# Kernel tuning notes

Measured on AMD Instinct MI355X. Metric: run time of the kernel, lower is better.

Reference implementation:

```python
import jax, jax.numpy as jnp
import numpy as np

B, S, D = 8, 1024, 1024
H = 16
HD = D // H  # 64
FF = 4 * D   # 4096
EPS = 1e-5


def layer_norm(x, g, b):
    mu = jnp.mean(x, axis=-1, keepdims=True)
    var = jnp.mean(jnp.square(x - mu), axis=-1, keepdims=True)
    return (x - mu) * jax.lax.rsqrt(var + EPS) * g + b


def setup_inputs() -> dict:
    key = jax.random.key(0)
    ks = jax.random.split(key, 16)
    s_in = 1.0 / np.sqrt(D)
    s_ff = 1.0 / np.sqrt(FF)
    return {
        "x": jax.random.normal(ks[0], (B, S, D), jnp.float32),
        "ln1_g": jnp.ones((D,), jnp.float32),
        "ln1_b": jnp.zeros((D,), jnp.float32),
        "ln2_g": jnp.ones((D,), jnp.float32),
        "ln2_b": jnp.zeros((D,), jnp.float32),
        # per-head projections stacked on a leading head axis: [H, D, HD]
        "Wq": jax.random.uniform(ks[1], (H, D, HD), jnp.float32, -s_in, s_in),
        "bq": jax.random.uniform(ks[2], (H, HD), jnp.float32, -s_in, s_in),
        "Wk": jax.random.uniform(ks[3], (H, D, HD), jnp.float32, -s_in, s_in),
        "bk": jax.random.uniform(ks[4], (H, HD), jnp.float32, -s_in, s_in),
        "Wv": jax.random.uniform(ks[5], (H, D, HD), jnp.float32, -s_in, s_in),
        "bv": jax.random.uniform(ks[6], (H, HD), jnp.float32, -s_in, s_in),
        "Wo": jax.random.uniform(ks[7], (D, D), jnp.float32, -s_in, s_in),
        "bo": jax.random.uniform(ks[8], (D,), jnp.float32, -s_in, s_in),
        "W1": jax.random.uniform(ks[9], (D, FF), jnp.float32, -s_in, s_in),
        "b1": jax.random.uniform(ks[10], (FF,), jnp.float32, -s_in, s_in),
        "W2": jax.random.uniform(ks[11], (FF, D), jnp.float32, -s_ff, s_ff),
        "b2": jax.random.uniform(ks[12], (D,), jnp.float32, -s_ff, s_ff),
    }


def attention(h, Wq, bq, Wk, bk, Wv, bv, Wo, bo):
    # h: [B,S,D] -> q/k/v: [B,H,S,HD]
    q = jnp.einsum("bsd,hdk->bhsk", h, Wq) + bq[None, :, None, :]
    k = jnp.einsum("bsd,hdk->bhsk", h, Wk) + bk[None, :, None, :]
    v = jnp.einsum("bsd,hdk->bhsk", h, Wv) + bv[None, :, None, :]
    scores = jnp.einsum("bhsk,bhtk->bhst", q, k) / jnp.sqrt(jnp.float32(HD))
    w = jax.nn.softmax(scores, axis=-1)  # [B,H,S,S]
    o = jnp.einsum("bhst,bhtk->bhsk", w, v)
    # concat heads (head order matches torch.cat over per-head outputs)
    o = o.transpose(0, 2, 1, 3).reshape(h.shape[0], h.shape[1], D)
    return o @ Wo + bo


def reference(x, ln1_g, ln1_b, ln2_g, ln2_b, Wq, bq, Wk, bk, Wv, bv, Wo, bo, W1, b1, W2, b2):
    h = layer_norm(x, ln1_g, ln1_b)
    x = x + attention(h, Wq, bq, Wk, bk, Wv, bv, Wo, bo)
    h2 = layer_norm(x, ln2_g, ln2_b)
    ff = jax.nn.gelu(h2 @ W1 + b1, approximate=False) @ W2 + b2  # dropout in eval = identity
    return x + ff
```

## Files before the change

### kernel.cpp

```cpp
#include <hip/hip_runtime.h>
#include <hip/hip_bf16.h>
#include <math.h>

#define DMODEL 1024
#define NH     16
#define HD     64
#define FFDIM  4096
#define SEQ    1024
#define BATCH  8
#define ROWS   (BATCH * SEQ)

typedef __bf16 bf16x8 __attribute__((ext_vector_type(8)));
typedef __bf16 bf16x4 __attribute__((ext_vector_type(4)));
typedef float  f32x4  __attribute__((ext_vector_type(4)));

__device__ __forceinline__ unsigned short f2bf(float f) {
  unsigned int u = __builtin_bit_cast(unsigned int, f);
  u += 0x7fff + ((u >> 16) & 1);
  return (unsigned short)(u >> 16);
}

__device__ __forceinline__ void gload_lds16(const void* g, void* l) {
  __builtin_amdgcn_global_load_lds(
      (const __attribute__((address_space(1))) unsigned int*)g,
      (__attribute__((address_space(3))) unsigned int*)l, 16, 0, 0);
}

__device__ __forceinline__ bf16x8 tr_read8(const unsigned short* p) {
  bf16x4 lo, hi;
  const __attribute__((address_space(3))) unsigned short* p3 =
      (const __attribute__((address_space(3))) unsigned short*)p;
  asm volatile("ds_read_b64_tr_b16 %0, %2\n\t"
               "ds_read_b64_tr_b16 %1, %2 offset:128"
               : "=v"(lo), "=v"(hi)
               : "v"(p3));
  return __builtin_shufflevector(lo, hi, 0, 1, 2, 3, 4, 5, 6, 7);
}

__global__ __launch_bounds__(256) void ln_bf16_kernel(
    const float* __restrict__ x, const float* __restrict__ g,
    const float* __restrict__ bta, unsigned short* __restrict__ out) {
  int row = blockIdx.x;
  int tid = threadIdx.x;
  int wid = tid >> 6, lane = tid & 63;
  const float4 v = ((const float4*)(x + (size_t)row * DMODEL))[tid];
  float s = v.x + v.y + v.z + v.w;
#pragma unroll
  for (int off = 32; off >= 1; off >>= 1) s += __shfl_xor(s, off, 64);
  __shared__ float red[8];
  if (lane == 0) red[wid] = s;
  __syncthreads();
  float mu = (red[0] + red[1] + red[2] + red[3]) * (1.0f / DMODEL);
  float4 d;
  d.x = v.x - mu; d.y = v.y - mu; d.z = v.z - mu; d.w = v.w - mu;
  float sq = d.x * d.x + d.y * d.y + d.z * d.z + d.w * d.w;
#pragma unroll
  for (int off = 32; off >= 1; off >>= 1) sq += __shfl_xor(sq, off, 64);
  if (lane == 0) red[4 + wid] = sq;
  __syncthreads();
  float var = (red[4] + red[5] + red[6] + red[7]) * (1.0f / DMODEL);
  float rs = rsqrtf(var + 1e-5f);
  const float4 gg = ((const float4*)g)[tid];
  const float4 bb = ((const float4*)bta)[tid];
  ushort4 o;
  o.x = f2bf(d.x * rs * gg.x + bb.x);
  o.y = f2bf(d.y * rs * gg.y + bb.y);
  o.z = f2bf(d.z * rs * gg.z + bb.z);
  o.w = f2bf(d.w * rs * gg.w + bb.w);
  ((ushort4*)(out + (size_t)row * DMODEL))[tid] = o;
}

__global__ __launch_bounds__(256) void transpose_f2b_kernel(
    const float* __restrict__ in, unsigned short* __restrict__ out,
    int R, int C, long long ibs, long long obs) {
  __shared__ float tile[64][65];
  int b = blockIdx.z;
  int r0 = blockIdx.y * 64, c0 = blockIdx.x * 64;
  const float* ip = in + (size_t)b * ibs;
  unsigned short* op = out + (size_t)b * obs;
  int tid = threadIdx.x;
  int rl = tid >> 4, cl = (tid & 15) * 4;
#pragma unroll
  for (int it = 0; it < 4; ++it) {
    int r = it * 16 + rl;
    float4 v = *(const float4*)(ip + (size_t)(r0 + r) * C + c0 + cl);
    tile[r][cl] = v.x; tile[r][cl + 1] = v.y;
    tile[r][cl + 2] = v.z; tile[r][cl + 3] = v.w;
  }
  __syncthreads();
#pragma unroll
  for (int it = 0; it < 4; ++it) {
    int c = it * 16 + rl;
    ushort4 o;
    o.x = f2bf(tile[cl + 0][c]); o.y = f2bf(tile[cl + 1][c]);
    o.z = f2bf(tile[cl + 2][c]); o.w = f2bf(tile[cl + 3][c]);
    *(ushort4*)(op + (size_t)(c0 + c) * R + r0 + cl) = o;
  }
}

__global__ __launch_bounds__(256) void transpose_v_kernel(
    const unsigned short* __restrict__ V, unsigned short* __restrict__ Vt) {
  __shared__ unsigned short tile[64][68];
  int bh = blockIdx.y;
  int b = bh >> 4, h = bh & 15;
  int t0 = blockIdx.x * 64;
  int tid = threadIdx.x;
  int rl = tid >> 4, cl = (tid & 15) * 4;
  const unsigned short* ip = V + ((size_t)(b * SEQ + t0)) * DMODEL + h * HD;
#pragma unroll
  for (int it = 0; it < 4; ++it) {
    int t = it * 16 + rl;
    ushort4 v = *(const ushort4*)(ip + (size_t)t * DMODEL + cl);
    tile[t][cl] = v.x; tile[t][cl + 1] = v.y;
    tile[t][cl + 2] = v.z; tile[t][cl + 3] = v.w;
  }
  __syncthreads();
  unsigned short* op = Vt + ((size_t)bh * HD) * SEQ + t0;
#pragma unroll
  for (int it = 0; it < 4; ++it) {
    int d = it * 16 + rl;
    ushort4 o;
    o.x = tile[cl + 0][d]; o.y = tile[cl + 1][d];
    o.z = tile[cl + 2][d]; o.w = tile[cl + 3][d];
    *(ushort4*)(op + (size_t)d * SEQ + cl) = o;
  }
}

#define QSCALE 0.18033688f

template <int EPI>
__global__ __launch_bounds__(512, 4) void gemmdb_kernel(
    const unsigned short* __restrict__ A, const unsigned short* __restrict__ Bt,
    const float* __restrict__ bias, const float* __restrict__ bias2,
    const float* __restrict__ bias3, const float* __restrict__ resid,
    unsigned short* __restrict__ outb, unsigned short* __restrict__ outb2,
    unsigned short* __restrict__ outb3, float* __restrict__ outf,
    int M, int N, int K, int NX) {
  __shared__ __align__(16) unsigned short As[2 * 128 * 64];
  __shared__ __align__(16) unsigned short Bs[2 * 128 * 64];

  const int tid = threadIdx.x;
  const int wid = tid >> 6, lane = tid & 63;
  const int l15 = lane & 15, l4 = lane >> 4;
  const int wm = wid >> 1, wn = wid & 1;

  const int id = (int)blockIdx.x;
  const int xcd = id & 7, j = id >> 3;
  const int w = j >> 6, l = j & 63;
  const int spx = (int)gridDim.x >> 9;
  const int nbx8 = NX >> 3;
  const int g = xcd * spx + w;
  const int by = (g / nbx8) * 8 + (l >> 3);
  const int bx = (g % nbx8) * 8 + (l & 7);

  const size_t KBY = (size_t)K * 2;

  const int rS = tid >> 3;
  const int cS = ((tid & 7) ^ (rS & 7)) << 4;
  const char* gA = (const char*)A + (size_t)(by * 128 + rS) * KBY + cS;
  const char* gB = (const char*)Bt + (size_t)(bx * 128 + rS) * KBY + cS;
  char* sA = (char*)As + tid * 16;
  char* sB = (char*)Bs + tid * 16;

  const int rsw = (l4 ^ (l15 & 7)) << 4;
  const char* aRd0 = (const char*)As + (wm * 32 + l15) * 128 + rsw;
  const char* aRd1 = (const char*)As + (wm * 32 + l15) * 128 + (rsw ^ 64);
  const char* bRd0 = (const char*)Bs + (wn * 64 + l15) * 128 + rsw;
  const char* bRd1 = (const char*)Bs + (wn * 64 + l15) * 128 + (rsw ^ 64);

  f32x4 acc[2][4];
  const f32x4 fz = {0.f, 0.f, 0.f, 0.f};
#pragma unroll
  for (int i = 0; i < 2; ++i)
#pragma unroll
    for (int j2 = 0; j2 < 4; ++j2) acc[i][j2] = fz;

  const int nt = K >> 6;

  gload_lds16(gA, sA);
  gload_lds16(gA + 64 * KBY, sA + 8192);
  gload_lds16(gB, sB);
  gload_lds16(gB + 64 * KBY, sB + 8192);
  asm volatile("s_waitcnt vmcnt(0)" ::: "memory");
  __builtin_amdgcn_sched_barrier(0);
  __builtin_amdgcn_s_barrier();
  __builtin_amdgcn_sched_barrier(0);

#pragma unroll 1
  for (int t = 0; t < nt; ++t) {
    const int cur = t & 1;
    if (t + 1 < nt) {
      const size_t ko = (size_t)(t + 1) << 7;
      const int nb = (cur ^ 1) << 14;
      gload_lds16(gA + ko, sA + nb);
      gload_lds16(gA + 64 * KBY + ko, sA + nb + 8192);
      gload_lds16(gB + ko, sB + nb);
      gload_lds16(gB + 64 * KBY + ko, sB + nb + 8192);
    }
    const int off = cur << 14;
#pragma unroll
    for (int kk = 0; kk < 2; ++kk) {
      const char* aR = (kk ? aRd1 : aRd0) + off;
      const char* bR = (kk ? bRd1 : bRd0) + off;
      bf16x8 afr[2], bfr[4];
#pragma unroll
      for (int ni = 0; ni < 4; ++ni) bfr[ni] = *(const bf16x8*)(bR + ni * 2048);
#pragma unroll
      for (int mi = 0; mi < 2; ++mi) afr[mi] = *(const bf16x8*)(aR + mi * 2048);
      __builtin_amdgcn_s_setprio(1);
#pragma unroll
      for (int mi = 0; mi < 2; ++mi)
#pragma unroll
        for (int ni = 0; ni < 4; ++ni)
          acc[mi][ni] = __builtin_amdgcn_mfma_f32_16x16x32_bf16(
              afr[mi], bfr[ni], acc[mi][ni], 0, 0, 0);
      __builtin_amdgcn_s_setprio(0);
    }
    asm volatile("s_waitcnt vmcnt(0)" ::: "memory");
    __builtin_amdgcn_sched_barrier(0);
    __builtin_amdgcn_s_barrier();
    __builtin_amdgcn_sched_barrier(0);
  }

  if (EPI == 5) {
    const int range = bx >> 3;
    const float* bp = (range == 0) ? bias : (range == 1) ? bias2 : bias3;
    unsigned short* op = (range == 0) ? outb : (range == 1) ? outb2 : outb3;
    const float scale = (range == 0) ? QSCALE : 1.0f;
#pragma unroll
    for (int mi = 0; mi < 2; ++mi) {
#pragma unroll
      for (int ni = 0; ni < 4; ++ni) {
        int colL = (bx & 7) * 128 + wn * 64 + ni * 16 + l15;
        float bn = bp[colL];
#pragma unroll
        for (int jj = 0; jj < 4; ++jj) {
          int row = by * 128 + wm * 32 + mi * 16 + l4 * 4 + jj;
          op[(size_t)row * 1024 + colL] = f2bf((acc[mi][ni][jj] + bn) * scale);
        }
      }
    }
  } else {
#pragma unroll
    for (int mi = 0; mi < 2; ++mi) {
#pragma unroll
      for (int ni = 0; ni < 4; ++ni) {
        int col = bx * 128 + wn * 64 + ni * 16 + l15;
        float bn = bias[col];
#pragma unroll
        for (int jj = 0; jj < 4; ++jj) {
          int row = by * 128 + wm * 32 + mi * 16 + l4 * 4 + jj;
          float v = acc[mi][ni][jj] + bn;
          if (EPI == 1) {
            outf[(size_t)row * N + col] = v + resid[(size_t)row * N + col];
          } else if (EPI == 2) {
            float gel = 0.5f * v * (1.0f + erff(v * 0.70710678118f));
            outb[(size_t)row * N + col] = f2bf(gel);
          } else {
            outb[(size_t)row * N + col] = f2bf(v);
          }
        }
      }
    }
  }
}

__global__ __launch_bounds__(256, 3) void attn_kernel(
    const unsigned short* __restrict__ Q, const unsigned short* __restrict__ K,
    const unsigned short* __restrict__ Vt, unsigned short* __restrict__ O) {
  __shared__ __align__(16) unsigned short Ks[128 * 64];
  __shared__ __align__(16) unsigned short Vs[64 * 128];
  __shared__ __align__(16) unsigned short Ps[4][128 * 16];
  int tid = threadIdx.x, wid = tid >> 6, lane = tid & 63;
  int l15 = lane & 15, l4 = lane >> 4;
  int sid = blockIdx.x;
  int aid = (sid & 7) * 256 + (sid >> 3);
  int bh = aid >> 4, qb = aid & 15;
  int b = bh >> 4, h = bh & 15;
  int q0 = qb * 64 + wid * 16;
  const f32x4 fz = {0.f, 0.f, 0.f, 0.f};

  const unsigned short* Qbase = Q + ((size_t)(b * SEQ + q0)) * DMODEL + h * HD;
  bf16x8 qf[2];
#pragma unroll
  for (int kh = 0; kh < 2; ++kh)
    qf[kh] = *(const bf16x8*)(Qbase + (size_t)l15 * DMODEL + kh * 32 + l4 * 8);

  f32x4 o[4];
#pragma unroll
  for (int i = 0; i < 4; ++i) o[i] = fz;
  float mrun[4], lrun[4];
#pragma unroll
  for (int j = 0; j < 4; ++j) { mrun[j] = -1e30f; lrun[j] = 0.0f; }

  const unsigned short* Kb = K + (size_t)b * SEQ * DMODEL + h * HD;
  const unsigned short* Vb = Vt + (size_t)bh * HD * SEQ;
  unsigned short* pbase = &Ps[wid][0];
  int krow = tid >> 3, kchunk = tid & 7;
  int vrow = tid >> 4, vchunk = tid & 15;

  for (int t0 = 0; t0 < SEQ; t0 += 128) {
    __syncthreads();
#pragma unroll
    for (int p = 0; p < 4; ++p) {
      int kr = p * 32 + krow;
      int kg = kchunk ^ (kr & 7);
      gload_lds16(Kb + (size_t)(t0 + kr) * DMODEL + kg * 8,
                  (char*)Ks + p * 4096 + tid * 16);
      int vr = p * 16 + vrow;
      int vg = vchunk ^ (vr & 7);
      gload_lds16(Vb + (size_t)vr * SEQ + t0 + vg * 8,
                  (char*)Vs + p * 4096 + tid * 16);
    }
    __syncthreads();
    f32x4 s[8];
#pragma unroll
    for (int ts = 0; ts < 8; ++ts) {
      int row = ts * 16 + l15;
      bf16x8 k0f = *(const bf16x8*)((const char*)Ks + row * 128 + ((l4) ^ (row & 7)) * 16);
      bf16x8 k1f = *(const bf16x8*)((const char*)Ks + row * 128 + ((4 + l4) ^ (row & 7)) * 16);
      s[ts] = __builtin_amdgcn_mfma_f32_16x16x32_bf16(qf[0], k0f, fz, 0, 0, 0);
      s[ts] = __builtin_amdgcn_mfma_f32_16x16x32_bf16(qf[1], k1f, s[ts], 0, 0, 0);
    }
#pragma unroll
    for (int j = 0; j < 4; ++j) {
      float tm = fmaxf(fmaxf(fmaxf(s[0][j], s[1][j]), fmaxf(s[2][j], s[3][j])),
                       fmaxf(fmaxf(s[4][j], s[5][j]), fmaxf(s[6][j], s[7][j])));
#pragma unroll
      for (int off = 8; off >= 1; off >>= 1) tm = fmaxf(tm, __shfl_xor(tm, off, 16));
      float mnew = fmaxf(mrun[j], tm);
      float alpha = __builtin_amdgcn_exp2f(mrun[j] - mnew);
      float ps = 0.0f;
#pragma unroll
      for (int ts = 0; ts < 8; ++ts) {
        float p = __builtin_amdgcn_exp2f(s[ts][j] - mnew);
        s[ts][j] = p;
        ps += p;
      }
#pragma unroll
      for (int off = 8; off >= 1; off >>= 1) ps += __shfl_xor(ps, off, 16);
      lrun[j] = lrun[j] * alpha + ps;
      mrun[j] = mnew;
#pragma unroll
      for (int d = 0; d < 4; ++d) o[d][j] *= alpha;
    }
#pragma unroll
    for (int ts = 0; ts < 8; ++ts) {
      ushort4 pk;
      pk.x = f2bf(s[ts][0]); pk.y = f2bf(s[ts][1]);
      pk.z = f2bf(s[ts][2]); pk.w = f2bf(s[ts][3]);
      *(ushort4*)((char*)pbase + (ts * 16 + l15) * 32 + l4 * 8) = pk;
    }
    asm volatile("s_waitcnt lgkmcnt(0)" ::: "memory");
    __builtin_amdgcn_sched_barrier(0);
#pragma unroll
    for (int kp = 0; kp < 4; ++kp) {
      bf16x8 pf = tr_read8(pbase + (kp * 32 + l4 * 8) * 16 + l15);
      asm volatile("s_waitcnt lgkmcnt(0)" ::: "memory");
      __builtin_amdgcn_sched_barrier(0);
#pragma unroll
      for (int d = 0; d < 4; ++d) {
        int vr = d * 16 + l15;
        int vphys = (kp * 4 + l4) ^ (vr & 7);
        bf16x8 vf = *(const bf16x8*)((const char*)Vs + vr * 256 + vphys * 16);
        o[d] = __builtin_amdgcn_mfma_f32_16x16x32_bf16(pf, vf, o[d], 0, 0, 0);
      }
    }
  }
  unsigned short* Ob = O + ((size_t)(b * SEQ + q0)) * DMODEL + h * HD;
#pragma unroll
  for (int j = 0; j < 4; ++j) {
    float inv = 1.0f / lrun[j];
#pragma unroll
    for (int d = 0; d < 4; ++d) {
      int row = l4 * 4 + j;
      Ob[(size_t)row * DMODEL + d * 16 + l15] = f2bf(o[d][j] * inv);
    }
  }
}

extern "C" void kernel_launch(void* const* d_in, const int* in_sizes, int n_in,
                              void* d_out, int out_size, void* d_ws, size_t ws_size,
                              hipStream_t stream) {
  (void)in_sizes; (void)n_in; (void)out_size; (void)ws_size;
  const float* x    = (const float*)d_in[0];
  const float* ln1g = (const float*)d_in[1];
  const float* ln1b = (const float*)d_in[2];
  const float* ln2g = (const float*)d_in[3];
  const float* ln2b = (const float*)d_in[4];
  const float* Wq   = (const float*)d_in[5];
  const float* bq   = (const float*)d_in[6];
  const float* Wk   = (const float*)d_in[7];
  const float* bk   = (const float*)d_in[8];
  const float* Wv   = (const float*)d_in[9];
  const float* bv   = (const float*)d_in[10];
  const float* Wo   = (const float*)d_in[11];
  const float* bo   = (const float*)d_in[12];
  const float* W1   = (const float*)d_in[13];
  const float* b1   = (const float*)d_in[14];
  const float* W2   = (const float*)d_in[15];
  const float* b2   = (const float*)d_in[16];
  float* out = (float*)d_out;

  char* ws = (char*)d_ws;
  const size_t MB = 1u << 20;
  unsigned short* wqT = (unsigned short*)(ws + 0 * MB);
  unsigned short* wkT = (unsigned short*)(ws + 2 * MB);
  unsigned short* wvT = (unsigned short*)(ws + 4 * MB);
  unsigned short* woT = (unsigned short*)(ws + 6 * MB);
  unsigned short* w1T = (unsigned short*)(ws + 8 * MB);
  unsigned short* w2T = (unsigned short*)(ws + 16 * MB);
  unsigned short* hb  = (unsigned short*)(ws + 24 * MB);
  unsigned short* Qb  = (unsigned short*)(ws + 40 * MB);
  unsigned short* Kb  = (unsigned short*)(ws + 56 * MB);
  unsigned short* Vb  = (unsigned short*)(ws + 72 * MB);
  unsigned short* Vt  = (unsigned short*)(ws + 88 * MB);
  unsigned short* Ob  = Vb;
  unsigned short* ff1 = (unsigned short*)(ws + 40 * MB);

  transpose_f2b_kernel<<<dim3(1, 16, 16), 256, 0, stream>>>(Wq, wqT, 1024, 64,
                                                            65536LL, 65536LL);
  transpose_f2b_kernel<<<dim3(1, 16, 16), 256, 0, stream>>>(Wk, wkT, 1024, 64,
                                                            65536LL, 65536LL);
  transpose_f2b_kernel<<<dim3(1, 16, 16), 256, 0, stream>>>(Wv, wvT, 1024, 64,
                                                            65536LL, 65536LL);
  transpose_f2b_kernel<<<dim3(16, 16, 1), 256, 0, stream>>>(Wo, woT, 1024, 1024, 0, 0);
  transpose_f2b_kernel<<<dim3(64, 16, 1), 256, 0, stream>>>(W1, w1T, 1024, 4096, 0, 0);
  transpose_f2b_kernel<<<dim3(16, 64, 1), 256, 0, stream>>>(W2, w2T, 4096, 1024, 0, 0);

  ln_bf16_kernel<<<dim3(ROWS), 256, 0, stream>>>(x, ln1g, ln1b, hb);

  gemmdb_kernel<5><<<dim3(1536), 512, 0, stream>>>(
      hb, wqT, bq, bk, bv, nullptr, Qb, Kb, Vb, nullptr, ROWS, 1024, DMODEL, 24);

  transpose_v_kernel<<<dim3(16, 128), 256, 0, stream>>>(Vb, Vt);

  attn_kernel<<<dim3(2048), 256, 0, stream>>>(Qb, Kb, Vt, Ob);

  gemmdb_kernel<1><<<dim3(512), 512, 0, stream>>>(
      Ob, woT, bo, nullptr, nullptr, x, nullptr, nullptr, nullptr, out,
      ROWS, DMODEL, DMODEL, 8);

  ln_bf16_kernel<<<dim3(ROWS), 256, 0, stream>>>(out, ln2g, ln2b, hb);

  gemmdb_kernel<2><<<dim3(2048), 512, 0, stream>>>(
      hb, w1T, b1, nullptr, nullptr, nullptr, ff1, nullptr, nullptr, nullptr,
      ROWS, FFDIM, DMODEL, 32);

  gemmdb_kernel<1><<<dim3(512), 512, 0, stream>>>(
      ff1, w2T, b2, nullptr, nullptr, out, nullptr, nullptr, nullptr, out,
      ROWS, DMODEL, FFDIM, 8);
}
```

Before: 392.8 us.

## Replace double-buffered GEMM with triple-buffered BK=32 ring pipeline and 256-thread blocks

```diff
diff --git a/kernel.cpp b/kernel.cpp
--- a/kernel.cpp
+++ b/kernel.cpp
@@ -35,6 +35,17 @@
                : "=v"(lo), "=v"(hi)
                : "v"(p3));
   return __builtin_shufflevector(lo, hi, 0, 1, 2, 3, 4, 5, 6, 7);
+}
+
+template <int N>
+__device__ __forceinline__ void wait_vm() {
+  if constexpr (N == 0)
+    asm volatile("s_waitcnt vmcnt(0)" ::: "memory");
+  else if constexpr (N == 3)
+    asm volatile("s_waitcnt vmcnt(3)" ::: "memory");
+  else
+    asm volatile("s_waitcnt vmcnt(4)" ::: "memory");
+  __builtin_amdgcn_sched_barrier(0);
 }
 
 __global__ __launch_bounds__(256) void ln_bf16_kernel(
@@ -128,16 +139,20 @@
 
 #define QSCALE 0.18033688f
 
-template <int EPI>
-__global__ __launch_bounds__(512, 4) void gemmdb_kernel(
+template <int BN, int EPI>
+__global__ __launch_bounds__(256, (BN == 64) ? 4 : 3) void gemmr3_kernel(
     const unsigned short* __restrict__ A, const unsigned short* __restrict__ Bt,
     const float* __restrict__ bias, const float* __restrict__ bias2,
     const float* __restrict__ bias3, const float* __restrict__ resid,
     unsigned short* __restrict__ outb, unsigned short* __restrict__ outb2,
     unsigned short* __restrict__ outb3, float* __restrict__ outf,
-    int M, int N, int K, int NX) {
-  __shared__ __align__(16) unsigned short As[2 * 128 * 64];
-  __shared__ __align__(16) unsigned short Bs[2 * 128 * 64];
+    int M, int N, int K, int NXS) {
+  constexpr int NFRAG = BN / 32;
+  constexpr int WN = BN / 2;
+  constexpr int LPT = (BN == 128) ? 4 : 3;
+  constexpr int BSLOT = BN * 64;
+  __shared__ __align__(16) unsigned short As[3 * 128 * 32];
+  __shared__ __align__(16) unsigned short Bs[3 * BN * 32];
 
   const int tid = threadIdx.x;
   const int wid = tid >> 6, lane = tid & 63;
@@ -148,78 +163,71 @@
   const int xcd = id & 7, j = id >> 3;
   const int w = j >> 6, l = j & 63;
   const int spx = (int)gridDim.x >> 9;
-  const int nbx8 = NX >> 3;
   const int g = xcd * spx + w;
-  const int by = (g / nbx8) * 8 + (l >> 3);
-  const int bx = (g % nbx8) * 8 + (l & 7);
+  const int by = (g / NXS) * 8 + (l >> 3);
+  const int bx = (g % NXS) * 8 + (l & 7);
 
   const size_t KBY = (size_t)K * 2;
 
-  const int rS = tid >> 3;
-  const int cS = ((tid & 7) ^ (rS & 7)) << 4;
+  const int rS = tid >> 2;
+  const int cS = ((tid & 3) ^ (rS & 3)) << 4;
   const char* gA = (const char*)A + (size_t)(by * 128 + rS) * KBY + cS;
-  const char* gB = (const char*)Bt + (size_t)(bx * 128 + rS) * KBY + cS;
+  const char* gB = (const char*)Bt + (size_t)(bx * BN + rS) * KBY + cS;
   char* sA = (char*)As + tid * 16;
   char* sB = (char*)Bs + tid * 16;
 
-  const int rsw = (l4 ^ (l15 & 7)) << 4;
-  const char* aRd0 = (const char*)As + (wm * 32 + l15) * 128 + rsw;
-  const char* aRd1 = (const char*)As + (wm * 32 + l15) * 128 + (rsw ^ 64);
-  const char* bRd0 = (const char*)Bs + (wn * 64 + l15) * 128 + rsw;
-  const char* bRd1 = (const char*)Bs + (wn * 64 + l15) * 128 + (rsw ^ 64);
-
-  f32x4 acc[2][4];
+  const int fsw = (l4 ^ (l15 & 3)) << 4;
+  const char* aRd = (const char*)As + (wm * 64 + l15) * 64 + fsw;
+  const char* bRd = (const char*)Bs + (wn * WN + l15) * 64 + fsw;
+
+  f32x4 acc[4][NFRAG];
   const f32x4 fz = {0.f, 0.f, 0.f, 0.f};
 #pragma unroll
-  for (int i = 0; i < 2; ++i)
-#pragma unroll
-    for (int j2 = 0; j2 < 4; ++j2) acc[i][j2] = fz;
-
-  const int nt = K >> 6;
-
-  gload_lds16(gA, sA);
-  gload_lds16(gA + 64 * KBY, sA + 8192);
-  gload_lds16(gB, sB);
-  gload_lds16(gB + 64 * KBY, sB + 8192);
-  asm volatile("s_waitcnt vmcnt(0)" ::: "memory");
-  __builtin_amdgcn_sched_barrier(0);
-  __builtin_amdgcn_s_barrier();
-  __builtin_amdgcn_sched_barrier(0);
-
+  for (int i = 0; i < 4; ++i)
+#pragma unroll
+    for (int n = 0; n < NFRAG; ++n) acc[i][n] = fz;
+
+  const int nt = K >> 5;
+
+#define STAGE(SLOT, T)                                                       \
+  do {                                                                       \
+    const size_t ko_ = (size_t)(T) * 64;                                     \
+    gload_lds16(gA + ko_, sA + (SLOT) * 8192);                               \
+    gload_lds16(gA + 64 * KBY + ko_, sA + (SLOT) * 8192 + 4096);             \
+    gload_lds16(gB + ko_, sB + (SLOT) * BSLOT);                              \
+    if constexpr (BN == 128)                                                 \
+      gload_lds16(gB + 64 * KBY + ko_, sB + (SLOT) * BSLOT + 4096);          \
+  } while (0)
+
+  STAGE(0, 0);
+  STAGE(1, 1);
+
+  int s = 0;
 #pragma unroll 1
   for (int t = 0; t < nt; ++t) {
-    const int cur = t & 1;
-    if (t + 1 < nt) {
-      const size_t ko = (size_t)(t + 1) << 7;
-      const int nb = (cur ^ 1) << 14;
-      gload_lds16(gA + ko, sA + nb);
-      gload_lds16(gA + 64 * KBY + ko, sA + nb + 8192);
-      gload_lds16(gB + ko, sB + nb);
-      gload_lds16(gB + 64 * KBY + ko, sB + nb + 8192);
-    }
-    const int off = cur << 14;
-#pragma unroll
-    for (int kk = 0; kk < 2; ++kk) {
-      const char* aR = (kk ? aRd1 : aRd0) + off;
-      const char* bR = (kk ? bRd1 : bRd0) + off;
-      bf16x8 afr[2], bfr[4];
-#pragma unroll
-      for (int ni = 0; ni < 4; ++ni) bfr[ni] = *(const bf16x8*)(bR + ni * 2048);
-#pragma unroll
-      for (int mi = 0; mi < 2; ++mi) afr[mi] = *(const bf16x8*)(aR + mi * 2048);
-      __builtin_amdgcn_s_setprio(1);
-#pragma unroll
-      for (int mi = 0; mi < 2; ++mi)
-#pragma unroll
-        for (int ni = 0; ni < 4; ++ni)
-          acc[mi][ni] = __builtin_amdgcn_mfma_f32_16x16x32_bf16(
-              afr[mi], bfr[ni], acc[mi][ni], 0, 0, 0);
-      __builtin_amdgcn_s_setprio(0);
-    }
-    asm volatile("s_waitcnt vmcnt(0)" ::: "memory");
-    __builtin_amdgcn_sched_barrier(0);
+    if (t + 1 < nt) wait_vm<LPT>(); else wait_vm<0>();
     __builtin_amdgcn_s_barrier();
     __builtin_amdgcn_sched_barrier(0);
+    const int s2 = (s == 0) ? 2 : s - 1;
+    if (t + 2 < nt) STAGE(s2, t + 2);
+    {
+      const char* aB = aRd + s * 8192;
+      const char* bB = bRd + s * BSLOT;
+      bf16x8 av[4], bv[NFRAG];
+#pragma unroll
+      for (int ni = 0; ni < NFRAG; ++ni) bv[ni] = *(const bf16x8*)(bB + ni * 1024);
+#pragma unroll
+      for (int mi = 0; mi < 4; ++mi) av[mi] = *(const bf16x8*)(aB + mi * 1024);
+      __builtin_amdgcn_s_setprio(1);
+#pragma unroll
+      for (int mi = 0; mi < 4; ++mi)
+#pragma unroll
+        for (int ni = 0; ni < NFRAG; ++ni)
+          acc[mi][ni] = __builtin_amdgcn_mfma_f32_16x16x32_bf16(
+              av[mi], bv[ni], acc[mi][ni], 0, 0, 0);
+      __builtin_amdgcn_s_setprio(0);
+    }
+    s = (s == 2) ? 0 : s + 1;
   }
 
   if (EPI == 5) {
@@ -228,28 +236,28 @@
     unsigned short* op = (range == 0) ? outb : (range == 1) ? outb2 : outb3;
     const float scale = (range == 0) ? QSCALE : 1.0f;
 #pragma unroll
-    for (int mi = 0; mi < 2; ++mi) {
-#pragma unroll
-      for (int ni = 0; ni < 4; ++ni) {
-        int colL = (bx & 7) * 128 + wn * 64 + ni * 16 + l15;
+    for (int mi = 0; mi < 4; ++mi) {
+#pragma unroll
+      for (int ni = 0; ni < NFRAG; ++ni) {
+        int colL = (bx & 7) * 128 + wn * WN + ni * 16 + l15;
         float bn = bp[colL];
 #pragma unroll
         for (int jj = 0; jj < 4; ++jj) {
-          int row = by * 128 + wm * 32 + mi * 16 + l4 * 4 + jj;
+          int row = by * 128 + wm * 64 + mi * 16 + l4 * 4 + jj;
           op[(size_t)row * 1024 + colL] = f2bf((acc[mi][ni][jj] + bn) * scale);
         }
       }
     }
   } else {
 #pragma unroll
-    for (int mi = 0; mi < 2; ++mi) {
-#pragma unroll
-      for (int ni = 0; ni < 4; ++ni) {
-        int col = bx * 128 + wn * 64 + ni * 16 + l15;
+    for (int mi = 0; mi < 4; ++mi) {
+#pragma unroll
+      for (int ni = 0; ni < NFRAG; ++ni) {
+        int col = bx * BN + wn * WN + ni * 16 + l15;
         float bn = bias[col];
 #pragma unroll
         for (int jj = 0; jj < 4; ++jj) {
-          int row = by * 128 + wm * 32 + mi * 16 + l4 * 4 + jj;
+          int row = by * 128 + wm * 64 + mi * 16 + l4 * 4 + jj;
           float v = acc[mi][ni][jj] + bn;
           if (EPI == 1) {
             outf[(size_t)row * N + col] = v + resid[(size_t)row * N + col];
@@ -263,6 +271,7 @@
       }
     }
   }
+#undef STAGE
 }
 
 __global__ __launch_bounds__(256, 3) void attn_kernel(
@@ -430,24 +439,24 @@
 
   ln_bf16_kernel<<<dim3(ROWS), 256, 0, stream>>>(x, ln1g, ln1b, hb);
 
-  gemmdb_kernel<5><<<dim3(1536), 512, 0, stream>>>(
-      hb, wqT, bq, bk, bv, nullptr, Qb, Kb, Vb, nullptr, ROWS, 1024, DMODEL, 24);
+  gemmr3_kernel<128, 5><<<dim3(1536), 256, 0, stream>>>(
+      hb, wqT, bq, bk, bv, nullptr, Qb, Kb, Vb, nullptr, ROWS, 1024, DMODEL, 3);
 
   transpose_v_kernel<<<dim3(16, 128), 256, 0, stream>>>(Vb, Vt);
 
   attn_kernel<<<dim3(2048), 256, 0, stream>>>(Qb, Kb, Vt, Ob);
 
-  gemmdb_kernel<1><<<dim3(512), 512, 0, stream>>>(
+  gemmr3_kernel<64, 1><<<dim3(1024), 256, 0, stream>>>(
       Ob, woT, bo, nullptr, nullptr, x, nullptr, nullptr, nullptr, out,
-      ROWS, DMODEL, DMODEL, 8);
+      ROWS, DMODEL, DMODEL, 2);
 
   ln_bf16_kernel<<<dim3(ROWS), 256, 0, stream>>>(out, ln2g, ln2b, hb);
 
-  gemmdb_kernel<2><<<dim3(2048), 512, 0, stream>>>(
+  gemmr3_kernel<128, 2><<<dim3(2048), 256, 0, stream>>>(
       hb, w1T, b1, nullptr, nullptr, nullptr, ff1, nullptr, nullptr, nullptr,
-      ROWS, FFDIM, DMODEL, 32);
-
-  gemmdb_kernel<1><<<dim3(512), 512, 0, stream>>>(
+      ROWS, FFDIM, DMODEL, 4);
+
+  gemmr3_kernel<64, 1><<<dim3(1024), 256, 0, stream>>>(
       ff1, w2T, b2, nullptr, nullptr, out, nullptr, nullptr, nullptr, out,
-      ROWS, DMODEL, FFDIM, 8);
-}
+      ROWS, DMODEL, FFDIM, 2);
+}
```

After: 446.1 us. 13.6% more time.

## Add 32x32x16 MFMA GEMM variant for QKV and FF1 projections

Applied to the files above, without the earlier changes.

```diff
diff --git a/kernel.cpp b/kernel.cpp
--- a/kernel.cpp
+++ b/kernel.cpp
@@ -13,6 +13,7 @@
 typedef __bf16 bf16x8 __attribute__((ext_vector_type(8)));
 typedef __bf16 bf16x4 __attribute__((ext_vector_type(4)));
 typedef float  f32x4  __attribute__((ext_vector_type(4)));
+typedef float  f32x16 __attribute__((ext_vector_type(16)));
 
 __device__ __forceinline__ unsigned short f2bf(float f) {
   unsigned int u = __builtin_bit_cast(unsigned int, f);
@@ -222,43 +223,153 @@
     __builtin_amdgcn_sched_barrier(0);
   }
 
+#pragma unroll
+  for (int mi = 0; mi < 2; ++mi) {
+#pragma unroll
+    for (int ni = 0; ni < 4; ++ni) {
+      int col = bx * 128 + wn * 64 + ni * 16 + l15;
+      float bn = bias[col];
+#pragma unroll
+      for (int jj = 0; jj < 4; ++jj) {
+        int row = by * 128 + wm * 32 + mi * 16 + l4 * 4 + jj;
+        float v = acc[mi][ni][jj] + bn;
+        if (EPI == 1) {
+          outf[(size_t)row * N + col] = v + resid[(size_t)row * N + col];
+        } else if (EPI == 2) {
+          float gel = 0.5f * v * (1.0f + erff(v * 0.70710678118f));
+          outb[(size_t)row * N + col] = f2bf(gel);
+        } else {
+          outb[(size_t)row * N + col] = f2bf(v);
+        }
+      }
+    }
+  }
+}
+
+template <int EPI>
+__global__ __launch_bounds__(512, 4) void gemm32_kernel(
+    const unsigned short* __restrict__ A, const unsigned short* __restrict__ Bt,
+    const float* __restrict__ bias, const float* __restrict__ bias2,
+    const float* __restrict__ bias3, const float* __restrict__ resid,
+    unsigned short* __restrict__ outb, unsigned short* __restrict__ outb2,
+    unsigned short* __restrict__ outb3, float* __restrict__ outf,
+    int M, int N, int K, int NX) {
+  __shared__ __align__(16) unsigned short As[2 * 128 * 64];
+  __shared__ __align__(16) unsigned short Bs[2 * 128 * 64];
+
+  const int tid = threadIdx.x;
+  const int wid = tid >> 6, lane = tid & 63;
+  const int l31 = lane & 31, l5 = lane >> 5;
+  const int wm = wid >> 1, wn = wid & 1;
+
+  const int id = (int)blockIdx.x;
+  const int xcd = id & 7, j = id >> 3;
+  const int w = j >> 6, l = j & 63;
+  const int spx = (int)gridDim.x >> 9;
+  const int nbx8 = NX >> 3;
+  const int g = xcd * spx + w;
+  const int by = (g / nbx8) * 8 + (l >> 3);
+  const int bx = (g % nbx8) * 8 + (l & 7);
+
+  const size_t KBY = (size_t)K * 2;
+
+  const int rS = tid >> 3;
+  const int cS = ((tid & 7) ^ (rS & 7)) << 4;
+  const char* gA = (const char*)A + (size_t)(by * 128 + rS) * KBY + cS;
+  const char* gB = (const char*)Bt + (size_t)(bx * 128 + rS) * KBY + cS;
+  char* sA = (char*)As + tid * 16;
+  char* sB = (char*)Bs + tid * 16;
+
+  const int rowA = wm * 32 + l31;
+  const int rowB = wn * 64 + l31;
+  const int aswz = rowA & 7;
+  const char* aRow = (const char*)As + rowA * 128;
+  const char* bRow = (const char*)Bs + rowB * 128;
+
+  f32x16 acc[2];
+#pragma unroll
+  for (int i = 0; i < 2; ++i)
+#pragma unroll
+    for (int r = 0; r < 16; ++r) acc[i][r] = 0.0f;
+
+  const int nt = K >> 6;
+
+  gload_lds16(gA, sA);
+  gload_lds16(gA + 64 * KBY, sA + 8192);
+  gload_lds16(gB, sB);
+  gload_lds16(gB + 64 * KBY, sB + 8192);
+  asm volatile("s_waitcnt vmcnt(0)" ::: "memory");
+  __builtin_amdgcn_sched_barrier(0);
+  __builtin_amdgcn_s_barrier();
+  __builtin_amdgcn_sched_barrier(0);
+
+#pragma unroll 1
+  for (int t = 0; t < nt; ++t) {
+    const int cur = t & 1;
+    if (t + 1 < nt) {
+      const size_t ko = (size_t)(t + 1) << 7;
+      const int nb = (cur ^ 1) << 14;
+      gload_lds16(gA + ko, sA + nb);
+      gload_lds16(gA + 64 * KBY + ko, sA + nb + 8192);
+      gload_lds16(gB + ko, sB + nb);
+      gload_lds16(gB + 64 * KBY + ko, sB + nb + 8192);
+    }
+    const int off = cur << 14;
+    {
+      bf16x8 av[4], bv[2][4];
+#pragma unroll
+      for (int kk = 0; kk < 4; ++kk) {
+        const int ch = ((((kk << 1) | l5) ^ aswz) << 4) + off;
+        av[kk] = *(const bf16x8*)(aRow + ch);
+        bv[0][kk] = *(const bf16x8*)(bRow + ch);
+        bv[1][kk] = *(const bf16x8*)(bRow + 4096 + ch);
+      }
+      __builtin_amdgcn_s_setprio(1);
+#pragma unroll
+      for (int kk = 0; kk < 4; ++kk)
+#pragma unroll
+        for (int ni = 0; ni < 2; ++ni)
+          acc[ni] = __builtin_amdgcn_mfma_f32_32x32x16_bf16(
+              av[kk], bv[ni][kk], acc[ni], 0, 0, 0);
+      __builtin_amdgcn_s_setprio(0);
+    }
+    asm volatile("s_waitcnt vmcnt(0)" ::: "memory");
+    __builtin_amdgcn_sched_barrier(0);
+    __builtin_amdgcn_s_barrier();
+    __builtin_amdgcn_sched_barrier(0);
+  }
+
   if (EPI == 5) {
     const int range = bx >> 3;
     const float* bp = (range == 0) ? bias : (range == 1) ? bias2 : bias3;
     unsigned short* op = (range == 0) ? outb : (range == 1) ? outb2 : outb3;
     const float scale = (range == 0) ? QSCALE : 1.0f;
 #pragma unroll
-    for (int mi = 0; mi < 2; ++mi) {
-#pragma unroll
-      for (int ni = 0; ni < 4; ++ni) {
-        int colL = (bx & 7) * 128 + wn * 64 + ni * 16 + l15;
-        float bn = bp[colL];
-#pragma unroll
-        for (int jj = 0; jj < 4; ++jj) {
-          int row = by * 128 + wm * 32 + mi * 16 + l4 * 4 + jj;
-          op[(size_t)row * 1024 + colL] = f2bf((acc[mi][ni][jj] + bn) * scale);
-        }
+    for (int ni = 0; ni < 2; ++ni) {
+      int colL = (bx & 7) * 128 + wn * 64 + ni * 32 + l31;
+      float bn = bp[colL];
+#pragma unroll
+      for (int reg = 0; reg < 16; ++reg) {
+        int row = by * 128 + wm * 32 + (reg & 3) + 8 * (reg >> 2) + 4 * l5;
+        op[(size_t)row * 1024 + colL] = f2bf((acc[ni][reg] + bn) * scale);
       }
     }
   } else {
 #pragma unroll
-    for (int mi = 0; mi < 2; ++mi) {
-#pragma unroll
-      for (int ni = 0; ni < 4; ++ni) {
-        int col = bx * 128 + wn * 64 + ni * 16 + l15;
-        float bn = bias[col];
-#pragma unroll
-        for (int jj = 0; jj < 4; ++jj) {
-          int row = by * 128 + wm * 32 + mi * 16 + l4 * 4 + jj;
-          float v = acc[mi][ni][jj] + bn;
-          if (EPI == 1) {
-            outf[(size_t)row * N + col] = v + resid[(size_t)row * N + col];
-          } else if (EPI == 2) {
-            float gel = 0.5f * v * (1.0f + erff(v * 0.70710678118f));
-            outb[(size_t)row * N + col] = f2bf(gel);
-          } else {
-            outb[(size_t)row * N + col] = f2bf(v);
-          }
+    for (int ni = 0; ni < 2; ++ni) {
+      int col = bx * 128 + wn * 64 + ni * 32 + l31;
+      float bn = bias[col];
+#pragma unroll
+      for (int reg = 0; reg < 16; ++reg) {
+        int row = by * 128 + wm * 32 + (reg & 3) + 8 * (reg >> 2) + 4 * l5;
+        float v = acc[ni][reg] + bn;
+        if (EPI == 1) {
+          outf[(size_t)row * N + col] = v + resid[(size_t)row * N + col];
+        } else if (EPI == 2) {
+          float gel = 0.5f * v * (1.0f + erff(v * 0.70710678118f));
+          outb[(size_t)row * N + col] = f2bf(gel);
+        } else {
+          outb[(size_t)row * N + col] = f2bf(v);
         }
       }
     }
@@ -430,7 +541,7 @@
 
   ln_bf16_kernel<<<dim3(ROWS), 256, 0, stream>>>(x, ln1g, ln1b, hb);
 
-  gemmdb_kernel<5><<<dim3(1536), 512, 0, stream>>>(
+  gemm32_kernel<5><<<dim3(1536), 512, 0, stream>>>(
       hb, wqT, bq, bk, bv, nullptr, Qb, Kb, Vb, nullptr, ROWS, 1024, DMODEL, 24);
 
   transpose_v_kernel<<<dim3(16, 128), 256, 0, stream>>>(Vb, Vt);
@@ -443,7 +554,7 @@
 
   ln_bf16_kernel<<<dim3(ROWS), 256, 0, stream>>>(out, ln2g, ln2b, hb);
 
-  gemmdb_kernel<2><<<dim3(2048), 512, 0, stream>>>(
+  gemm32_kernel<2><<<dim3(2048), 512, 0, stream>>>(
       hb, w1T, b1, nullptr, nullptr, nullptr, ff1, nullptr, nullptr, nullptr,
       ROWS, FFDIM, DMODEL, 32);
 
```

Result: slower. 411.7 us (+4.8%).
